# Kernel optimization log

Hardware: AMD Instinct MI355X
Metric: run time of the kernel (lower is better)

The kernel has to match this reference:

```python
import jax, jax.numpy as jnp
import numpy as np

N = 4096      # num_nodes
F = 256       # node_dim
K = 4         # num_heads
FP = 64       # out_dim per head
P_EDGE = 0.008  # edge probability (~33 avg degree)


def setup_inputs() -> dict:
    key = jax.random.key(0)
    k1, k2, k3, k4, k5 = jax.random.split(key, 5)
    x = jax.random.normal(k1, (N, F), dtype=jnp.float32)
    # binary adjacency mask with self loops so every row has a neighbor
    adj = (jax.random.uniform(k2, (N, N)) < P_EDGE).astype(jnp.float32)
    mask = jnp.maximum(adj, jnp.eye(N, dtype=jnp.float32))
    batch = jnp.zeros((N,), dtype=jnp.int32)  # unused (is_final_layer=False)
    # xavier-style init for W (node_dim -> K*FP) and attention vectors
    w_scale = np.sqrt(2.0 / (F + K * FP)).astype(np.float32)
    W = jax.random.normal(k3, (F, K * FP), dtype=jnp.float32) * w_scale
    b = jnp.zeros((K * FP,), dtype=jnp.float32)
    a_scale = np.sqrt(2.0 / (K * FP + 1)).astype(np.float32)
    a_left = jax.random.normal(k4, (1, K, FP), dtype=jnp.float32) * a_scale
    a_right = jax.random.normal(k5, (1, K, FP), dtype=jnp.float32) * a_scale
    return {"x": x, "mask": mask, "batch": batch, "W": W, "b": b,
            "a_left": a_left, "a_right": a_right}


def reference(x, mask, batch, W, b, a_left, a_right):
    # dropout prob = 0.0 (eval mode) -> identity
    x_proj = (x @ W + b).reshape(N, K, FP)                 # (N,K,F')
    score_src = (x_proj * a_left).sum(axis=-1)             # (N,K)
    score_tgt = (x_proj * a_right).sum(axis=-1)            # (N,K)
    score = score_src[:, None, :] + score_tgt[None, :, :]  # (N,N,K)
    score = jax.nn.leaky_relu(score, negative_slope=0.2)
    # non-standard global mean/std normalization (torch .std() is unbiased)
    score = (score - score.mean()) / score.std(ddof=1)
    score = jnp.exp(score)
    m = mask[:, :, None]                                   # (N,N,1)
    denom = (score * m).sum(axis=1, keepdims=True)         # (N,1,K)
    aij = (score / denom) * m                              # (N,N,K)
    attention = jnp.transpose(aij, (2, 0, 1))              # (K,N,N)
    h_prime = jnp.einsum('knm,mkf->nkf', attention, x_proj)  # (N,K,F')
    h_prime = jax.nn.elu(h_prime)
    # is_final_layer=False -> concat heads
    return h_prime.reshape(N, K * FP)
```

## Files before the change

kernel.cpp:

```cpp
#include <hip/hip_runtime.h>
#include <hip/hip_bf16.h>
#include <math.h>

#define NN 4096
#define FF 256
#define KH 4
#define FP 64
#define NCOL 256
#define MAXNBR 512
#define MOM_BLOCKS 2048

__device__ __forceinline__ float bits2f(unsigned b) {
    union { unsigned u; float f; } c; c.u = b << 16; return c.f;
}

#define OFF_SUMS   0
#define OFF_FLAG   16
#define OFF_PART   128
#define OFF_WF     4194432
#define OFF_BIAS   4456576
#define OFF_AL     4457600
#define OFF_AR     4458624
#define OFF_XP     4459648
#define OFF_SRC    8653952
#define OFF_TGT    8719488
#define OFF_NBR    8785024
#define OFF_CNT    12979328

__global__ void k_detect(const unsigned* __restrict__ mask_raw,
                         int* __restrict__ flag) {
    if (threadIdx.x == 0)
        *flag = (mask_raw[0] == 0x3F800000u) ? 1 : 0;
}

__global__ __launch_bounds__(256) void k_cvt_w(
        const void* __restrict__ Wr, const void* __restrict__ br,
        const void* __restrict__ alr, const void* __restrict__ arr,
        const int* __restrict__ flag,
        float* __restrict__ WF, float* __restrict__ bias_f,
        float* __restrict__ al_f, float* __restrict__ ar_f) {
    int idx = blockIdx.x * 256 + threadIdx.x;
    int fl = *flag;
    WF[idx] = fl ? ((const float*)Wr)[idx] : bits2f(((const unsigned short*)Wr)[idx]);
    if (idx < NCOL) {
        bias_f[idx] = fl ? ((const float*)br)[idx]  : bits2f(((const unsigned short*)br)[idx]);
        al_f[idx]   = fl ? ((const float*)alr)[idx] : bits2f(((const unsigned short*)alr)[idx]);
        ar_f[idx]   = fl ? ((const float*)arr)[idx] : bits2f(((const unsigned short*)arr)[idx]);
    }
}

__global__ __launch_bounds__(256) void k_rows(
        const void* __restrict__ mask, const int* __restrict__ flag,
        unsigned short* __restrict__ nbr_g, int* __restrict__ cnt_g) {
    __shared__ int cnt;
    int n = blockIdx.x;
    if (threadIdx.x == 0) cnt = 0;
    __syncthreads();
    unsigned short* rn = nbr_g + (size_t)n * MAXNBR;
    if (*flag) {
        const uint4* p = (const uint4*)((const float*)mask + (size_t)n * NN);
        for (int i = threadIdx.x; i < NN / 4; i += 256) {
            uint4 v = p[i]; int base = i * 4;
            if (v.x) { int s = atomicAdd(&cnt, 1); if (s < MAXNBR) rn[s] = base + 0; }
            if (v.y) { int s = atomicAdd(&cnt, 1); if (s < MAXNBR) rn[s] = base + 1; }
            if (v.z) { int s = atomicAdd(&cnt, 1); if (s < MAXNBR) rn[s] = base + 2; }
            if (v.w) { int s = atomicAdd(&cnt, 1); if (s < MAXNBR) rn[s] = base + 3; }
        }
    } else {
        const uint4* p = (const uint4*)((const unsigned short*)mask + (size_t)n * NN);
        for (int i = threadIdx.x; i < NN / 8; i += 256) {
            uint4 v = p[i]; int base = i * 8;
            if (v.x & 0xFFFFu) { int s = atomicAdd(&cnt, 1); if (s < MAXNBR) rn[s] = base + 0; }
            if (v.x >> 16)     { int s = atomicAdd(&cnt, 1); if (s < MAXNBR) rn[s] = base + 1; }
            if (v.y & 0xFFFFu) { int s = atomicAdd(&cnt, 1); if (s < MAXNBR) rn[s] = base + 2; }
            if (v.y >> 16)     { int s = atomicAdd(&cnt, 1); if (s < MAXNBR) rn[s] = base + 3; }
            if (v.z & 0xFFFFu) { int s = atomicAdd(&cnt, 1); if (s < MAXNBR) rn[s] = base + 4; }
            if (v.z >> 16)     { int s = atomicAdd(&cnt, 1); if (s < MAXNBR) rn[s] = base + 5; }
            if (v.w & 0xFFFFu) { int s = atomicAdd(&cnt, 1); if (s < MAXNBR) rn[s] = base + 6; }
            if (v.w >> 16)     { int s = atomicAdd(&cnt, 1); if (s < MAXNBR) rn[s] = base + 7; }
        }
    }
    __syncthreads();
    if (threadIdx.x == 0) cnt_g[n] = cnt < MAXNBR ? cnt : MAXNBR;
}

__global__ __launch_bounds__(256) void gat_gemm_valu(
        const void* __restrict__ xr, const int* __restrict__ flag,
        const float* __restrict__ WF, const float* __restrict__ bias,
        const float* __restrict__ alf, const float* __restrict__ arf,
        float* __restrict__ xp, float* __restrict__ src, float* __restrict__ tgt) {
    __shared__ float4 xs[8][64];
    int n0 = blockIdx.x * 8;
    if (*flag) {
        const float4* xq = (const float4*)xr;
        for (int t = threadIdx.x; t < 512; t += 256) {
            int r = t >> 6, q = t & 63;
            xs[r][q] = xq[(size_t)(n0 + r) * 64 + q];
        }
    } else {
        const ushort4* xq = (const ushort4*)xr;
        for (int t = threadIdx.x; t < 512; t += 256) {
            int r = t >> 6, q = t & 63;
            ushort4 u = xq[(size_t)(n0 + r) * 64 + q];
            float4 v; v.x = bits2f(u.x); v.y = bits2f(u.y); v.z = bits2f(u.z); v.w = bits2f(u.w);
            xs[r][q] = v;
        }
    }
    __syncthreads();
    int c = threadIdx.x;
    float acc[8] = {};
    for (int kk = 0; kk < 64; ++kk) {
        float w0 = WF[(4 * kk + 0) * NCOL + c];
        float w1 = WF[(4 * kk + 1) * NCOL + c];
        float w2 = WF[(4 * kk + 2) * NCOL + c];
        float w3 = WF[(4 * kk + 3) * NCOL + c];
        #pragma unroll
        for (int r = 0; r < 8; ++r) {
            float4 xv = xs[r][kk];
            acc[r] += xv.x * w0 + xv.y * w1 + xv.z * w2 + xv.w * w3;
        }
    }
    float bv = bias[c];
    float alv = alf[c], arv = arf[c];
    int wave = threadIdx.x >> 6;
    int lane = threadIdx.x & 63;
    #pragma unroll
    for (int r = 0; r < 8; ++r) {
        float o = acc[r] + bv;
        xp[(size_t)(n0 + r) * NCOL + c] = o;
        float sr = o * alv, tr = o * arv;
        #pragma unroll
        for (int off = 32; off; off >>= 1) {
            sr += __shfl_down(sr, off, 64);
            tr += __shfl_down(tr, off, 64);
        }
        if (lane == 0) {
            src[(n0 + r) * KH + wave] = sr;
            tgt[(n0 + r) * KH + wave] = tr;
        }
    }
}

__global__ __launch_bounds__(256) void k_moments_a(
        const float* __restrict__ src, const float* __restrict__ tgt,
        double2* __restrict__ partials) {
    const int total = NN * NN;
    const int stride = MOM_BLOCKS * 256;
    float s1 = 0.f, s2 = 0.f;
    for (int p = blockIdx.x * 256 + threadIdx.x; p < total; p += stride) {
        int n = p >> 12, m = p & 4095;
        float4 sv = ((const float4*)src)[n];
        float4 tv = ((const float4*)tgt)[m];
        float v0 = sv.x + tv.x; v0 = v0 > 0.f ? v0 : 0.2f * v0;
        float v1 = sv.y + tv.y; v1 = v1 > 0.f ? v1 : 0.2f * v1;
        float v2 = sv.z + tv.z; v2 = v2 > 0.f ? v2 : 0.2f * v2;
        float v3 = sv.w + tv.w; v3 = v3 > 0.f ? v3 : 0.2f * v3;
        s1 += v0 + v1 + v2 + v3;
        s2 += v0 * v0 + v1 * v1 + v2 * v2 + v3 * v3;
    }
    __shared__ double l1[256], l2[256];
    l1[threadIdx.x] = (double)s1;
    l2[threadIdx.x] = (double)s2;
    __syncthreads();
    for (int off = 128; off; off >>= 1) {
        if (threadIdx.x < off) {
            l1[threadIdx.x] += l1[threadIdx.x + off];
            l2[threadIdx.x] += l2[threadIdx.x + off];
        }
        __syncthreads();
    }
    if (threadIdx.x == 0) {
        double2 pr; pr.x = l1[0]; pr.y = l2[0];
        partials[blockIdx.x] = pr;
    }
}

__global__ __launch_bounds__(256) void k_moments_b(
        const double2* __restrict__ partials, double* __restrict__ sums) {
    double a = 0.0, b = 0.0;
    for (int i = threadIdx.x; i < MOM_BLOCKS; i += 256) {
        double2 pr = partials[i];
        a += pr.x; b += pr.y;
    }
    __shared__ double l1[256], l2[256];
    l1[threadIdx.x] = a;
    l2[threadIdx.x] = b;
    __syncthreads();
    for (int off = 128; off; off >>= 1) {
        if (threadIdx.x < off) {
            l1[threadIdx.x] += l1[threadIdx.x + off];
            l2[threadIdx.x] += l2[threadIdx.x + off];
        }
        __syncthreads();
    }
    if (threadIdx.x == 0) {
        sums[0] = l1[0];
        sums[1] = l2[0];
    }
}

__global__ __launch_bounds__(256) void gat_aggregate(
        const unsigned short* __restrict__ nbr_g, const int* __restrict__ cnt_g,
        const float* __restrict__ xp,
        const float* __restrict__ src, const float* __restrict__ tgt,
        const double* __restrict__ sums,
        float* __restrict__ out) {
    __shared__ unsigned short snbr[MAXNBR];
    __shared__ float pls[MAXNBR * KH];
    __shared__ float invden[KH];
    int n = blockIdx.x;
    int c = cnt_g[n];
    for (int j = threadIdx.x; j < c; j += 256) snbr[j] = nbr_g[(size_t)n * MAXNBR + j];
    __syncthreads();

    double s = sums[0], ss = sums[1];
    const double tot = (double)NN * (double)NN * (double)KH;
    float mu = (float)(s / tot);
    float inv_sigma = (float)(1.0 / sqrt((ss - s * s / tot) / (tot - 1.0)));

    for (int t = threadIdx.x; t < c * KH; t += 256) {
        int j = t >> 2, k = t & 3;
        int m = snbr[j];
        float v = src[n * KH + k] + tgt[m * KH + k];
        v = v > 0.f ? v : 0.2f * v;
        pls[j * KH + k] = expf((v - mu) * inv_sigma);
    }
    __syncthreads();
    if (threadIdx.x < KH) {
        float d = 0.f;
        for (int j = 0; j < c; ++j) d += pls[j * KH + threadIdx.x];
        invden[threadIdx.x] = 1.0f / d;
    }
    __syncthreads();

    int col = threadIdx.x;
    int k = col >> 6;
    float acc = 0.f;
    for (int j = 0; j < c; ++j) {
        acc += pls[j * KH + k] * xp[(size_t)snbr[j] * NCOL + col];
    }
    acc *= invden[k];
    float o = acc > 0.f ? acc : expm1f(acc);
    out[(size_t)n * NCOL + col] = o;
}

extern "C" void kernel_launch(void* const* d_in, const int* in_sizes, int n_in,
                              void* d_out, int out_size, void* d_ws, size_t ws_size,
                              hipStream_t stream) {
    const void* x    = d_in[0];
    const void* mask = d_in[1];
    const void* W    = d_in[3];
    const void* b    = d_in[4];
    const void* al   = d_in[5];
    const void* ar   = d_in[6];

    char* ws = (char*)d_ws;
    double* sums = (double*)(ws + OFF_SUMS);
    int* flag = (int*)(ws + OFF_FLAG);
    double2* part = (double2*)(ws + OFF_PART);
    float* WF   = (float*)(ws + OFF_WF);
    float* bias = (float*)(ws + OFF_BIAS);
    float* alf  = (float*)(ws + OFF_AL);
    float* arf  = (float*)(ws + OFF_AR);
    float* xp   = (float*)(ws + OFF_XP);
    float* src  = (float*)(ws + OFF_SRC);
    float* tgt  = (float*)(ws + OFF_TGT);
    unsigned short* nbr = (unsigned short*)(ws + OFF_NBR);
    int* cntg = (int*)(ws + OFF_CNT);

    k_detect<<<1, 64, 0, stream>>>((const unsigned*)mask, flag);
    k_cvt_w<<<256, 256, 0, stream>>>(W, b, al, ar, flag, WF, bias, alf, arf);
    k_rows<<<4096, 256, 0, stream>>>(mask, flag, nbr, cntg);
    gat_gemm_valu<<<512, 256, 0, stream>>>(x, flag, WF, bias, alf, arf, xp, src, tgt);
    k_moments_a<<<MOM_BLOCKS, 256, 0, stream>>>(src, tgt, part);
    k_moments_b<<<1, 256, 0, stream>>>(part, sums);
    gat_aggregate<<<4096, 256, 0, stream>>>(nbr, cntg, xp, src, tgt, sums,
                                            (float*)d_out);
}
```

Measured before the change: 170.4 us.

## Fuse mask scan into aggregate and drop separate detect/convert kernels

```diff
diff --git a/kernel.cpp b/kernel.cpp
--- a/kernel.cpp
+++ b/kernel.cpp
@@ -13,85 +13,25 @@
 __device__ __forceinline__ float bits2f(unsigned b) {
     union { unsigned u; float f; } c; c.u = b << 16; return c.f;
 }
+__device__ __forceinline__ int is_fp32(const void* mask) {
+    return ((const unsigned*)mask)[0] == 0x3F800000u;
+}
 
 #define OFF_SUMS   0
-#define OFF_FLAG   16
 #define OFF_PART   128
-#define OFF_WF     4194432
-#define OFF_BIAS   4456576
-#define OFF_AL     4457600
-#define OFF_AR     4458624
-#define OFF_XP     4459648
-#define OFF_SRC    8653952
-#define OFF_TGT    8719488
-#define OFF_NBR    8785024
-#define OFF_CNT    12979328
-
-__global__ void k_detect(const unsigned* __restrict__ mask_raw,
-                         int* __restrict__ flag) {
-    if (threadIdx.x == 0)
-        *flag = (mask_raw[0] == 0x3F800000u) ? 1 : 0;
-}
-
-__global__ __launch_bounds__(256) void k_cvt_w(
+#define OFF_XP     65536
+#define OFF_SRC    4259840
+#define OFF_TGT    4325376
+
+__global__ __launch_bounds__(256) void gat_gemm_valu(
+        const void* __restrict__ xr, const void* __restrict__ mask,
         const void* __restrict__ Wr, const void* __restrict__ br,
         const void* __restrict__ alr, const void* __restrict__ arr,
-        const int* __restrict__ flag,
-        float* __restrict__ WF, float* __restrict__ bias_f,
-        float* __restrict__ al_f, float* __restrict__ ar_f) {
-    int idx = blockIdx.x * 256 + threadIdx.x;
-    int fl = *flag;
-    WF[idx] = fl ? ((const float*)Wr)[idx] : bits2f(((const unsigned short*)Wr)[idx]);
-    if (idx < NCOL) {
-        bias_f[idx] = fl ? ((const float*)br)[idx]  : bits2f(((const unsigned short*)br)[idx]);
-        al_f[idx]   = fl ? ((const float*)alr)[idx] : bits2f(((const unsigned short*)alr)[idx]);
-        ar_f[idx]   = fl ? ((const float*)arr)[idx] : bits2f(((const unsigned short*)arr)[idx]);
-    }
-}
-
-__global__ __launch_bounds__(256) void k_rows(
-        const void* __restrict__ mask, const int* __restrict__ flag,
-        unsigned short* __restrict__ nbr_g, int* __restrict__ cnt_g) {
-    __shared__ int cnt;
-    int n = blockIdx.x;
-    if (threadIdx.x == 0) cnt = 0;
-    __syncthreads();
-    unsigned short* rn = nbr_g + (size_t)n * MAXNBR;
-    if (*flag) {
-        const uint4* p = (const uint4*)((const float*)mask + (size_t)n * NN);
-        for (int i = threadIdx.x; i < NN / 4; i += 256) {
-            uint4 v = p[i]; int base = i * 4;
-            if (v.x) { int s = atomicAdd(&cnt, 1); if (s < MAXNBR) rn[s] = base + 0; }
-            if (v.y) { int s = atomicAdd(&cnt, 1); if (s < MAXNBR) rn[s] = base + 1; }
-            if (v.z) { int s = atomicAdd(&cnt, 1); if (s < MAXNBR) rn[s] = base + 2; }
-            if (v.w) { int s = atomicAdd(&cnt, 1); if (s < MAXNBR) rn[s] = base + 3; }
-        }
-    } else {
-        const uint4* p = (const uint4*)((const unsigned short*)mask + (size_t)n * NN);
-        for (int i = threadIdx.x; i < NN / 8; i += 256) {
-            uint4 v = p[i]; int base = i * 8;
-            if (v.x & 0xFFFFu) { int s = atomicAdd(&cnt, 1); if (s < MAXNBR) rn[s] = base + 0; }
-            if (v.x >> 16)     { int s = atomicAdd(&cnt, 1); if (s < MAXNBR) rn[s] = base + 1; }
-            if (v.y & 0xFFFFu) { int s = atomicAdd(&cnt, 1); if (s < MAXNBR) rn[s] = base + 2; }
-            if (v.y >> 16)     { int s = atomicAdd(&cnt, 1); if (s < MAXNBR) rn[s] = base + 3; }
-            if (v.z & 0xFFFFu) { int s = atomicAdd(&cnt, 1); if (s < MAXNBR) rn[s] = base + 4; }
-            if (v.z >> 16)     { int s = atomicAdd(&cnt, 1); if (s < MAXNBR) rn[s] = base + 5; }
-            if (v.w & 0xFFFFu) { int s = atomicAdd(&cnt, 1); if (s < MAXNBR) rn[s] = base + 6; }
-            if (v.w >> 16)     { int s = atomicAdd(&cnt, 1); if (s < MAXNBR) rn[s] = base + 7; }
-        }
-    }
-    __syncthreads();
-    if (threadIdx.x == 0) cnt_g[n] = cnt < MAXNBR ? cnt : MAXNBR;
-}
-
-__global__ __launch_bounds__(256) void gat_gemm_valu(
-        const void* __restrict__ xr, const int* __restrict__ flag,
-        const float* __restrict__ WF, const float* __restrict__ bias,
-        const float* __restrict__ alf, const float* __restrict__ arf,
         float* __restrict__ xp, float* __restrict__ src, float* __restrict__ tgt) {
+    const int fl = is_fp32(mask);
     __shared__ float4 xs[8][64];
     int n0 = blockIdx.x * 8;
-    if (*flag) {
+    if (fl) {
         const float4* xq = (const float4*)xr;
         for (int t = threadIdx.x; t < 512; t += 256) {
             int r = t >> 6, q = t & 63;
@@ -109,19 +49,43 @@
     __syncthreads();
     int c = threadIdx.x;
     float acc[8] = {};
-    for (int kk = 0; kk < 64; ++kk) {
-        float w0 = WF[(4 * kk + 0) * NCOL + c];
-        float w1 = WF[(4 * kk + 1) * NCOL + c];
-        float w2 = WF[(4 * kk + 2) * NCOL + c];
-        float w3 = WF[(4 * kk + 3) * NCOL + c];
-        #pragma unroll
-        for (int r = 0; r < 8; ++r) {
-            float4 xv = xs[r][kk];
-            acc[r] += xv.x * w0 + xv.y * w1 + xv.z * w2 + xv.w * w3;
-        }
-    }
-    float bv = bias[c];
-    float alv = alf[c], arv = arf[c];
+    if (fl) {
+        const float* WF = (const float*)Wr;
+        for (int kk = 0; kk < 64; ++kk) {
+            float w0 = WF[(4 * kk + 0) * NCOL + c];
+            float w1 = WF[(4 * kk + 1) * NCOL + c];
+            float w2 = WF[(4 * kk + 2) * NCOL + c];
+            float w3 = WF[(4 * kk + 3) * NCOL + c];
+            #pragma unroll
+            for (int r = 0; r < 8; ++r) {
+                float4 xv = xs[r][kk];
+                acc[r] += xv.x * w0 + xv.y * w1 + xv.z * w2 + xv.w * w3;
+            }
+        }
+    } else {
+        const unsigned short* WB = (const unsigned short*)Wr;
+        for (int kk = 0; kk < 64; ++kk) {
+            float w0 = bits2f(WB[(4 * kk + 0) * NCOL + c]);
+            float w1 = bits2f(WB[(4 * kk + 1) * NCOL + c]);
+            float w2 = bits2f(WB[(4 * kk + 2) * NCOL + c]);
+            float w3 = bits2f(WB[(4 * kk + 3) * NCOL + c]);
+            #pragma unroll
+            for (int r = 0; r < 8; ++r) {
+                float4 xv = xs[r][kk];
+                acc[r] += xv.x * w0 + xv.y * w1 + xv.z * w2 + xv.w * w3;
+            }
+        }
+    }
+    float bv, alv, arv;
+    if (fl) {
+        bv  = ((const float*)br)[c];
+        alv = ((const float*)alr)[c];
+        arv = ((const float*)arr)[c];
+    } else {
+        bv  = bits2f(((const unsigned short*)br)[c]);
+        alv = bits2f(((const unsigned short*)alr)[c]);
+        arv = bits2f(((const unsigned short*)arr)[c]);
+    }
     int wave = threadIdx.x >> 6;
     int lane = threadIdx.x & 63;
     #pragma unroll
@@ -200,7 +164,7 @@
 }
 
 __global__ __launch_bounds__(256) void gat_aggregate(
-        const unsigned short* __restrict__ nbr_g, const int* __restrict__ cnt_g,
+        const void* __restrict__ mask,
         const float* __restrict__ xp,
         const float* __restrict__ src, const float* __restrict__ tgt,
         const double* __restrict__ sums,
@@ -208,10 +172,37 @@
     __shared__ unsigned short snbr[MAXNBR];
     __shared__ float pls[MAXNBR * KH];
     __shared__ float invden[KH];
+    __shared__ int cnt;
+    const int fl = is_fp32(mask);
     int n = blockIdx.x;
-    int c = cnt_g[n];
-    for (int j = threadIdx.x; j < c; j += 256) snbr[j] = nbr_g[(size_t)n * MAXNBR + j];
-    __syncthreads();
+    if (threadIdx.x == 0) cnt = 0;
+    __syncthreads();
+
+    if (fl) {
+        const uint4* p = (const uint4*)((const float*)mask + (size_t)n * NN);
+        for (int i = threadIdx.x; i < NN / 4; i += 256) {
+            uint4 v = p[i]; int base = i * 4;
+            if (v.x) { int s = atomicAdd(&cnt, 1); if (s < MAXNBR) snbr[s] = base + 0; }
+            if (v.y) { int s = atomicAdd(&cnt, 1); if (s < MAXNBR) snbr[s] = base + 1; }
+            if (v.z) { int s = atomicAdd(&cnt, 1); if (s < MAXNBR) snbr[s] = base + 2; }
+            if (v.w) { int s = atomicAdd(&cnt, 1); if (s < MAXNBR) snbr[s] = base + 3; }
+        }
+    } else {
+        const uint4* p = (const uint4*)((const unsigned short*)mask + (size_t)n * NN);
+        for (int i = threadIdx.x; i < NN / 8; i += 256) {
+            uint4 v = p[i]; int base = i * 8;
+            if (v.x & 0xFFFFu) { int s = atomicAdd(&cnt, 1); if (s < MAXNBR) snbr[s] = base + 0; }
+            if (v.x >> 16)     { int s = atomicAdd(&cnt, 1); if (s < MAXNBR) snbr[s] = base + 1; }
+            if (v.y & 0xFFFFu) { int s = atomicAdd(&cnt, 1); if (s < MAXNBR) snbr[s] = base + 2; }
+            if (v.y >> 16)     { int s = atomicAdd(&cnt, 1); if (s < MAXNBR) snbr[s] = base + 3; }
+            if (v.z & 0xFFFFu) { int s = atomicAdd(&cnt, 1); if (s < MAXNBR) snbr[s] = base + 4; }
+            if (v.z >> 16)     { int s = atomicAdd(&cnt, 1); if (s < MAXNBR) snbr[s] = base + 5; }
+            if (v.w & 0xFFFFu) { int s = atomicAdd(&cnt, 1); if (s < MAXNBR) snbr[s] = base + 6; }
+            if (v.w >> 16)     { int s = atomicAdd(&cnt, 1); if (s < MAXNBR) snbr[s] = base + 7; }
+        }
+    }
+    __syncthreads();
+    int c = cnt < MAXNBR ? cnt : MAXNBR;
 
     double s = sums[0], ss = sums[1];
     const double tot = (double)NN * (double)NN * (double)KH;
@@ -256,24 +247,14 @@
 
     char* ws = (char*)d_ws;
     double* sums = (double*)(ws + OFF_SUMS);
-    int* flag = (int*)(ws + OFF_FLAG);
     double2* part = (double2*)(ws + OFF_PART);
-    float* WF   = (float*)(ws + OFF_WF);
-    float* bias = (float*)(ws + OFF_BIAS);
-    float* alf  = (float*)(ws + OFF_AL);
-    float* arf  = (float*)(ws + OFF_AR);
     float* xp   = (float*)(ws + OFF_XP);
     float* src  = (float*)(ws + OFF_SRC);
     float* tgt  = (float*)(ws + OFF_TGT);
-    unsigned short* nbr = (unsigned short*)(ws + OFF_NBR);
-    int* cntg = (int*)(ws + OFF_CNT);
-
-    k_detect<<<1, 64, 0, stream>>>((const unsigned*)mask, flag);
-    k_cvt_w<<<256, 256, 0, stream>>>(W, b, al, ar, flag, WF, bias, alf, arf);
-    k_rows<<<4096, 256, 0, stream>>>(mask, flag, nbr, cntg);
-    gat_gemm_valu<<<512, 256, 0, stream>>>(x, flag, WF, bias, alf, arf, xp, src, tgt);
+
+    gat_gemm_valu<<<512, 256, 0, stream>>>(x, mask, W, b, al, ar, xp, src, tgt);
     k_moments_a<<<MOM_BLOCKS, 256, 0, stream>>>(src, tgt, part);
     k_moments_b<<<1, 256, 0, stream>>>(part, sums);
-    gat_aggregate<<<4096, 256, 0, stream>>>(nbr, cntg, xp, src, tgt, sums,
+    gat_aggregate<<<4096, 256, 0, stream>>>(mask, xp, src, tgt, sums,
                                             (float*)d_out);
 }
```

New measurement: 164.0 us. 3.8% less time.
